# Optimization experiments

Measured on AMD Instinct MI355X. Metric: run time of the kernel, lower is better.

## Reference

```python
import jax, jax.numpy as jnp
import numpy as np


def setup_inputs() -> dict:
    key = jax.random.key(0)
    k1, k2, k3 = jax.random.split(key, 3)
    b, c, h, w = 4, 64, 64, 64
    content = jax.random.normal(k1, (b, c, h, w), dtype=jnp.float32)
    content_s = jax.random.normal(k2, (b, c, h, w), dtype=jnp.float32)
    style = jax.random.normal(k3, (b, c, h, w), dtype=jnp.float32)
    return {"content": content, "content_s": content_s, "style": style}


def reference(content, content_s, style):
    b, c, h, w = content.shape
    hw = h * w
    Fc = content.reshape(b, c, hw)      # [b, c, HW]
    Fs = content_s.reshape(b, c, hw)    # [b, c, HW]
    Fst = style.reshape(b, c, hw)       # [b, c, HW]
    # S[b, q, k] = sum_c Fc[b, c, q] * Fs[b, c, k]  (Fc transposed as in torch)
    S = jnp.einsum('bcq,bck->bqk', Fc, Fs)
    S = jax.nn.softmax(S, axis=-1)
    # O = style @ S^T : O[b, c, q] = sum_k Fst[b, c, k] * S[b, q, k]
    O = jnp.einsum('bck,bqk->bcq', Fst, S).reshape(b, c, h, w)
    return jnp.concatenate((content, O), axis=1)
```

## Files before the change

kernel.cpp:

```cpp
#include <hip/hip_runtime.h>
#include <math.h>


#define Bb 4
#define Cc 64
#define HWs 4096
#define SPLITS 4
#define TILES_PER_SPLIT 16
#define RLOG2E 1.44269504088896340736f

typedef _Float16 half8 __attribute__((ext_vector_type(8)));
typedef _Float16 half4 __attribute__((ext_vector_type(4)));
typedef float floatx4 __attribute__((ext_vector_type(4)));

__global__ __launch_bounds__(256) void prep_k(const float* __restrict__ content,
                                              const float* __restrict__ Fs,
                                              const float* __restrict__ Fst,
                                              float* __restrict__ out,
                                              _Float16* __restrict__ Kt,
                                              _Float16* __restrict__ Vt) {
    const int bid = blockIdx.x;
    const int t = threadIdx.x;
    if (bid < 1024) {
        int i4 = bid * 256 + t;
        const float4* c4 = (const float4*)content;
        const float4* v4 = (const float4*)Fst;
        float4* o4 = (float4*)out;
        int b = i4 >> 16, rem = i4 & 65535;
        o4[(size_t)b * 131072 + rem] = c4[i4];
        float4 v = v4[i4];
        half4 h;
        h[0] = (_Float16)v.x; h[1] = (_Float16)v.y;
        h[2] = (_Float16)v.z; h[3] = (_Float16)v.w;
        *(half4*)(Vt + (size_t)i4 * 4) = h;
    } else {
        __shared__ _Float16 T[16][72];
        int e = bid - 1024;
        int b = e >> 8;
        int hw0 = (e & 255) * 16;
        const float* sb = Fs + (size_t)b * Cc * HWs;
        {
            int c = t >> 2, x4 = (t & 3) * 4;
            float4 v = *(const float4*)(sb + (size_t)c * HWs + hw0 + x4);
            T[x4 + 0][c] = (_Float16)v.x;
            T[x4 + 1][c] = (_Float16)v.y;
            T[x4 + 2][c] = (_Float16)v.z;
            T[x4 + 3][c] = (_Float16)v.w;
        }
        __syncthreads();
        if (t < 128) {
            int row = t >> 3, g = t & 7;
            _Float16* db = Kt + (size_t)b * HWs * Cc;
            *(half8*)(db + (size_t)(hw0 + row) * Cc + g * 8) = *(half8*)&T[row][g * 8];
        }
    }
}

__global__ __launch_bounds__(256, 2) void attn_k(const float* __restrict__ Fc,
                                                 const _Float16* __restrict__ Kt,
                                                 const _Float16* __restrict__ Vt,
                                                 _Float16* __restrict__ Opart,
                                                 float2* __restrict__ ml) {
    const int tid  = threadIdx.x;
    const int w    = tid >> 6;
    const int lane = tid & 63;
    const int quad = lane >> 4;
    const int l15  = lane & 15;
    const int qg = blockIdx.x & 31;
    const int b  = (blockIdx.x >> 5) & 3;
    const int s  = blockIdx.x >> 7;
    const int k0base = s * TILES_PER_SPLIT * 64;
    const int qA = qg * 128 + w * 32 + l15;
    const int qB = qA + 16;

    __shared__ _Float16 Kl[2][64 * 64];
    __shared__ _Float16 Vl[2][64 * 64];
    __shared__ _Float16 Ps[4][32][72];

    const float*    Fcb = Fc + (size_t)b * Cc * HWs;
    const _Float16* Kb  = Kt + (size_t)b * HWs * Cc;
    const _Float16* Vb  = Vt + (size_t)b * Cc * HWs;

    const bool isK  = tid < 128;
    const int  sl   = tid & 127;
    const int  srow = sl >> 3;
    const int  sjg  = sl & 7;
    const int  ssw  = (sjg ^ (srow & 7)) * 8;

    half8 qf[2][2];
    #pragma unroll
    for (int j = 0; j < 8; ++j) {
        qf[0][0][j] = (_Float16)(Fcb[(size_t)(quad * 8 + j) * HWs + qA] * RLOG2E);
        qf[0][1][j] = (_Float16)(Fcb[(size_t)(32 + quad * 8 + j) * HWs + qA] * RLOG2E);
        qf[1][0][j] = (_Float16)(Fcb[(size_t)(quad * 8 + j) * HWs + qB] * RLOG2E);
        qf[1][1][j] = (_Float16)(Fcb[(size_t)(32 + quad * 8 + j) * HWs + qB] * RLOG2E);
    }

    half8 st[4];
    auto stage_load = [&](int kt) {
        int kk0 = k0base + kt * 64;
        #pragma unroll
        for (int i = 0; i < 4; ++i) {
            int row = srow + 16 * i;
            if (isK) st[i] = *(const half8*)(Kb + (size_t)(kk0 + row) * 64 + sjg * 8);
            else     st[i] = *(const half8*)(Vb + (size_t)row * HWs + kk0 + sjg * 8);
        }
    };
    auto stage_write = [&](int p) {
        #pragma unroll
        for (int i = 0; i < 4; ++i) {
            int row = srow + 16 * i;
            if (isK) *(half8*)&Kl[p][row * 64 + ssw] = st[i];
            else     *(half8*)&Vl[p][row * 64 + ssw] = st[i];
        }
    };

    floatx4 acc[2][4];
    #pragma unroll
    for (int g = 0; g < 2; ++g)
        #pragma unroll
        for (int m = 0; m < 4; ++m) acc[g][m] = (floatx4)(0.0f);
    float m_run[2] = {-INFINITY, -INFINITY};
    float lsum[2] = {0.0f, 0.0f};

    stage_load(0);
    stage_write(0);
    stage_load(1);
    __syncthreads();

    const int swl = (l15 & 7);
    for (int kt = 0; kt < TILES_PER_SPLIT; ++kt) {
        const int p = kt & 1;
        if (kt + 1 < TILES_PER_SPLIT) stage_write(p ^ 1);
        if (kt + 2 < TILES_PER_SPLIT) stage_load(kt + 2);

        half8 ka[4][2];
        #pragma unroll
        for (int m = 0; m < 4; ++m)
            #pragma unroll
            for (int cs = 0; cs < 2; ++cs)
                ka[m][cs] = *(const half8*)&Kl[p][(m * 16 + l15) * 64 + (((cs * 4 + quad) ^ swl) * 8)];

        floatx4 sv[2][4];
        #pragma unroll
        for (int m = 0; m < 4; ++m) {
            #pragma unroll
            for (int g = 0; g < 2; ++g) {
                sv[g][m] = __builtin_amdgcn_mfma_f32_16x16x32_f16(ka[m][0], qf[g][0], (floatx4)(0.0f), 0, 0, 0);
                sv[g][m] = __builtin_amdgcn_mfma_f32_16x16x32_f16(ka[m][1], qf[g][1], sv[g][m], 0, 0, 0);
            }
        }

        half8 va[4][2];
        #pragma unroll
        for (int m = 0; m < 4; ++m)
            #pragma unroll
            for (int ks = 0; ks < 2; ++ks)
                va[m][ks] = *(const half8*)&Vl[p][(m * 16 + l15) * 64 + (((ks * 4 + quad) ^ swl) * 8)];

        half8 pb[2][2];
        #pragma unroll
        for (int g = 0; g < 2; ++g) {
            float mx = -INFINITY;
            #pragma unroll
            for (int m = 0; m < 4; ++m)
                #pragma unroll
                for (int r = 0; r < 4; ++r) mx = fmaxf(mx, sv[g][m][r]);
            mx = fmaxf(mx, __shfl_xor(mx, 16));
            mx = fmaxf(mx, __shfl_xor(mx, 32));
            float m_new = fmaxf(m_run[g], mx);
            float alpha = exp2f(m_run[g] - m_new);
            m_run[g] = m_new;
            float part = 0.0f;
            #pragma unroll
            for (int m = 0; m < 4; ++m)
                #pragma unroll
                for (int r = 0; r < 4; ++r) {
                    float e = exp2f(sv[g][m][r] - m_new);
                    sv[g][m][r] = e;
                    part += e;
                }
            lsum[g] = lsum[g] * alpha + part;
            #pragma unroll
            for (int m = 0; m < 4; ++m)
                #pragma unroll
                for (int r = 0; r < 4; ++r) acc[g][m][r] *= alpha;

            #pragma unroll
            for (int m = 0; m < 4; ++m) {
                half4 pp;
                pp[0] = (_Float16)sv[g][m][0]; pp[1] = (_Float16)sv[g][m][1];
                pp[2] = (_Float16)sv[g][m][2]; pp[3] = (_Float16)sv[g][m][3];
                *(half4*)&Ps[w][g * 16 + l15][m * 16 + quad * 4] = pp;
            }
            pb[g][0] = *(half8*)&Ps[w][g * 16 + l15][quad * 8];
            pb[g][1] = *(half8*)&Ps[w][g * 16 + l15][32 + quad * 8];
        }

        #pragma unroll
        for (int m = 0; m < 4; ++m)
            #pragma unroll
            for (int g = 0; g < 2; ++g) {
                acc[g][m] = __builtin_amdgcn_mfma_f32_16x16x32_f16(va[m][0], pb[g][0], acc[g][m], 0, 0, 0);
                acc[g][m] = __builtin_amdgcn_mfma_f32_16x16x32_f16(va[m][1], pb[g][1], acc[g][m], 0, 0, 0);
            }

        __syncthreads();
    }

    _Float16* op = Opart + (((size_t)s * Bb + b) * Cc) * HWs;
    #pragma unroll
    for (int g = 0; g < 2; ++g) {
        lsum[g] += __shfl_xor(lsum[g], 16);
        lsum[g] += __shfl_xor(lsum[g], 32);
        int q = (g == 0) ? qA : qB;
        #pragma unroll
        for (int m = 0; m < 4; ++m)
            #pragma unroll
            for (int r = 0; r < 4; ++r) {
                int c = m * 16 + quad * 4 + r;
                op[(size_t)c * HWs + q] = (_Float16)acc[g][m][r];
            }
        if (quad == 0)
            ml[((size_t)b * HWs + q) * SPLITS + s] = make_float2(m_run[g], lsum[g]);
    }
}

__global__ __launch_bounds__(256) void combine_k(const _Float16* __restrict__ Opart,
                                                 const float2* __restrict__ ml,
                                                 float* __restrict__ out) {
    int idx = blockIdx.x * 256 + threadIdx.x;
    int q = idx & 4095;
    int c = (idx >> 12) & 63;
    int b = idx >> 18;
    const float2* mlp = ml + ((size_t)b * HWs + q) * SPLITS;
    float2 mls[SPLITS];
    #pragma unroll
    for (int s = 0; s < SPLITS; ++s) mls[s] = mlp[s];
    float M = -INFINITY;
    #pragma unroll
    for (int s = 0; s < SPLITS; ++s) M = fmaxf(M, mls[s].x);
    float l = 0.0f, wgt[SPLITS];
    #pragma unroll
    for (int s = 0; s < SPLITS; ++s) {
        wgt[s] = exp2f(mls[s].x - M);
        l += wgt[s] * mls[s].y;
    }
    float o = 0.0f;
    #pragma unroll
    for (int s = 0; s < SPLITS; ++s)
        o += wgt[s] * (float)Opart[(((size_t)s * Bb + b) * Cc + c) * HWs + q];
    out[((size_t)b * 2 * Cc + Cc + c) * HWs + q] = o / l;
}

extern "C" void kernel_launch(void* const* d_in, const int* in_sizes, int n_in,
                              void* d_out, int out_size, void* d_ws, size_t ws_size,
                              hipStream_t stream) {
    const float* content   = (const float*)d_in[0];
    const float* content_s = (const float*)d_in[1];
    const float* style     = (const float*)d_in[2];
    float* out = (float*)d_out;

    _Float16* Kt = (_Float16*)d_ws;
    _Float16* Vt = Kt + (size_t)Bb * HWs * Cc;
    _Float16* Opart = Vt + (size_t)Bb * Cc * HWs;
    float2*   ml = (float2*)(Opart + (size_t)SPLITS * Bb * Cc * HWs);

    prep_k<<<dim3(2048), dim3(256), 0, stream>>>(content, content_s, style, out, Kt, Vt);
    attn_k<<<dim3(SPLITS * Bb * 32), dim3(256), 0, stream>>>(content, Kt, Vt, Opart, ml);
    combine_k<<<dim3(4096), dim3(256), 0, stream>>>(Opart, ml, out);
}
```

Before: 109.1 us.

## Restructure flash-attention inner loop with lazy rescale, register P transpose, more splits

Removes the LDS round-trip for the probability tile by packing exp values to fp16 and transposing them with permlane32/permlane16 swaps. The running-max rescale is now skipped unless the max grows past a threshold, and the row sum is computed on the matrix cores by multiplying against a ones vector. Occupancy is raised to 4 blocks per SM and the key dimension is split into 8 pieces when the workspace is large enough. The intent is to cut ALU, LDS and sync overhead in the softmax. In exchange it adds more partial outputs for the combine kernel and relies on fp16 range holding under the deferred rescale.

Result: slower. 112.7 us, median of 2 (+3.2%).

```diff
diff --git a/kernel.cpp b/kernel.cpp
--- a/kernel.cpp
+++ b/kernel.cpp
@@ -5,13 +5,13 @@
 #define Bb 4
 #define Cc 64
 #define HWs 4096
-#define SPLITS 4
-#define TILES_PER_SPLIT 16
 #define RLOG2E 1.44269504088896340736f
+#define DEFER_THR 6.0f
 
 typedef _Float16 half8 __attribute__((ext_vector_type(8)));
 typedef _Float16 half4 __attribute__((ext_vector_type(4)));
 typedef float floatx4 __attribute__((ext_vector_type(4)));
+typedef unsigned uint2v __attribute__((ext_vector_type(2)));
 
 __global__ __launch_bounds__(256) void prep_k(const float* __restrict__ content,
                                               const float* __restrict__ Fs,
@@ -56,11 +56,13 @@
     }
 }
 
-__global__ __launch_bounds__(256, 2) void attn_k(const float* __restrict__ Fc,
+template <int NS>
+__global__ __launch_bounds__(256, 4) void attn_k(const float* __restrict__ Fc,
                                                  const _Float16* __restrict__ Kt,
                                                  const _Float16* __restrict__ Vt,
                                                  _Float16* __restrict__ Opart,
                                                  float2* __restrict__ ml) {
+    constexpr int TPS = 64 / NS;
     const int tid  = threadIdx.x;
     const int w    = tid >> 6;
     const int lane = tid & 63;
@@ -69,13 +71,12 @@
     const int qg = blockIdx.x & 31;
     const int b  = (blockIdx.x >> 5) & 3;
     const int s  = blockIdx.x >> 7;
-    const int k0base = s * TILES_PER_SPLIT * 64;
+    const int k0base = s * TPS * 64;
     const int qA = qg * 128 + w * 32 + l15;
     const int qB = qA + 16;
 
     __shared__ _Float16 Kl[2][64 * 64];
     __shared__ _Float16 Vl[2][64 * 64];
-    __shared__ _Float16 Ps[4][32][72];
 
     const float*    Fcb = Fc + (size_t)b * Cc * HWs;
     const _Float16* Kb  = Kt + (size_t)b * HWs * Cc;
@@ -116,12 +117,18 @@
     };
 
     floatx4 acc[2][4];
-    #pragma unroll
-    for (int g = 0; g < 2; ++g)
+    floatx4 accl[2];
+    #pragma unroll
+    for (int g = 0; g < 2; ++g) {
+        accl[g] = (floatx4)(0.0f);
         #pragma unroll
         for (int m = 0; m < 4; ++m) acc[g][m] = (floatx4)(0.0f);
+    }
     float m_run[2] = {-INFINITY, -INFINITY};
-    float lsum[2] = {0.0f, 0.0f};
+
+    half8 vone;
+    #pragma unroll
+    for (int j = 0; j < 8; ++j) vone[j] = (_Float16)1.0f;
 
     stage_load(0);
     stage_write(0);
@@ -129,90 +136,99 @@
     __syncthreads();
 
     const int swl = (l15 & 7);
-    for (int kt = 0; kt < TILES_PER_SPLIT; ++kt) {
+    for (int kt = 0; kt < TPS; ++kt) {
         const int p = kt & 1;
-        if (kt + 1 < TILES_PER_SPLIT) stage_write(p ^ 1);
-        if (kt + 2 < TILES_PER_SPLIT) stage_load(kt + 2);
-
-        half8 ka[4][2];
-        #pragma unroll
-        for (int m = 0; m < 4; ++m)
-            #pragma unroll
-            for (int cs = 0; cs < 2; ++cs)
-                ka[m][cs] = *(const half8*)&Kl[p][(m * 16 + l15) * 64 + (((cs * 4 + quad) ^ swl) * 8)];
+        if (kt + 1 < TPS) stage_write(p ^ 1);
+        if (kt + 2 < TPS) stage_load(kt + 2);
 
         floatx4 sv[2][4];
         #pragma unroll
         for (int m = 0; m < 4; ++m) {
-            #pragma unroll
-            for (int g = 0; g < 2; ++g) {
-                sv[g][m] = __builtin_amdgcn_mfma_f32_16x16x32_f16(ka[m][0], qf[g][0], (floatx4)(0.0f), 0, 0, 0);
-                sv[g][m] = __builtin_amdgcn_mfma_f32_16x16x32_f16(ka[m][1], qf[g][1], sv[g][m], 0, 0, 0);
-            }
-        }
-
-        half8 va[4][2];
-        #pragma unroll
-        for (int m = 0; m < 4; ++m)
-            #pragma unroll
-            for (int ks = 0; ks < 2; ++ks)
-                va[m][ks] = *(const half8*)&Vl[p][(m * 16 + l15) * 64 + (((ks * 4 + quad) ^ swl) * 8)];
+            const half8 ka0 = *(const half8*)&Kl[p][(m * 16 + l15) * 64 + ((quad ^ swl) * 8)];
+            const half8 ka1 = *(const half8*)&Kl[p][(m * 16 + l15) * 64 + (((4 + quad) ^ swl) * 8)];
+            sv[0][m] = __builtin_amdgcn_mfma_f32_16x16x32_f16(ka0, qf[0][0], (floatx4)(0.0f), 0, 0, 0);
+            sv[0][m] = __builtin_amdgcn_mfma_f32_16x16x32_f16(ka1, qf[0][1], sv[0][m], 0, 0, 0);
+            sv[1][m] = __builtin_amdgcn_mfma_f32_16x16x32_f16(ka0, qf[1][0], (floatx4)(0.0f), 0, 0, 0);
+            sv[1][m] = __builtin_amdgcn_mfma_f32_16x16x32_f16(ka1, qf[1][1], sv[1][m], 0, 0, 0);
+        }
 
         half8 pb[2][2];
         #pragma unroll
         for (int g = 0; g < 2; ++g) {
-            float mx = -INFINITY;
+            float mx = sv[g][0][0];
             #pragma unroll
             for (int m = 0; m < 4; ++m)
                 #pragma unroll
                 for (int r = 0; r < 4; ++r) mx = fmaxf(mx, sv[g][m][r]);
-            mx = fmaxf(mx, __shfl_xor(mx, 16));
-            mx = fmaxf(mx, __shfl_xor(mx, 32));
-            float m_new = fmaxf(m_run[g], mx);
-            float alpha = exp2f(m_run[g] - m_new);
-            m_run[g] = m_new;
-            float part = 0.0f;
-            #pragma unroll
-            for (int m = 0; m < 4; ++m)
+            {
+                unsigned mu = __float_as_uint(mx);
+                uint2v t32 = __builtin_amdgcn_permlane32_swap(mu, mu, false, false);
+                mx = fmaxf(__uint_as_float(t32[0]), __uint_as_float(t32[1]));
+                mu = __float_as_uint(mx);
+                uint2v t16 = __builtin_amdgcn_permlane16_swap(mu, mu, false, false);
+                mx = fmaxf(__uint_as_float(t16[0]), __uint_as_float(t16[1]));
+            }
+            if (!__all(mx - m_run[g] <= DEFER_THR)) {
+                float m_new = fmaxf(m_run[g], mx);
+                float alpha = exp2f(m_run[g] - m_new);
+                m_run[g] = m_new;
                 #pragma unroll
-                for (int r = 0; r < 4; ++r) {
-                    float e = exp2f(sv[g][m][r] - m_new);
-                    sv[g][m][r] = e;
-                    part += e;
-                }
-            lsum[g] = lsum[g] * alpha + part;
-            #pragma unroll
-            for (int m = 0; m < 4; ++m)
-                #pragma unroll
-                for (int r = 0; r < 4; ++r) acc[g][m][r] *= alpha;
-
+                for (int m = 0; m < 4; ++m) acc[g][m] *= alpha;
+                accl[g] *= alpha;
+            }
+            const float mb = m_run[g];
+            unsigned Ap[4], Bp[4];
             #pragma unroll
             for (int m = 0; m < 4; ++m) {
-                half4 pp;
-                pp[0] = (_Float16)sv[g][m][0]; pp[1] = (_Float16)sv[g][m][1];
-                pp[2] = (_Float16)sv[g][m][2]; pp[3] = (_Float16)sv[g][m][3];
-                *(half4*)&Ps[w][g * 16 + l15][m * 16 + quad * 4] = pp;
-            }
-            pb[g][0] = *(half8*)&Ps[w][g * 16 + l15][quad * 8];
-            pb[g][1] = *(half8*)&Ps[w][g * 16 + l15][32 + quad * 8];
-        }
-
-        #pragma unroll
-        for (int m = 0; m < 4; ++m)
-            #pragma unroll
-            for (int g = 0; g < 2; ++g) {
-                acc[g][m] = __builtin_amdgcn_mfma_f32_16x16x32_f16(va[m][0], pb[g][0], acc[g][m], 0, 0, 0);
-                acc[g][m] = __builtin_amdgcn_mfma_f32_16x16x32_f16(va[m][1], pb[g][1], acc[g][m], 0, 0, 0);
-            }
+                float e0 = exp2f(sv[g][m][0] - mb);
+                float e1 = exp2f(sv[g][m][1] - mb);
+                float e2 = exp2f(sv[g][m][2] - mb);
+                float e3 = exp2f(sv[g][m][3] - mb);
+                Ap[m] = __builtin_bit_cast(unsigned, __builtin_amdgcn_cvt_pkrtz(e0, e1));
+                Bp[m] = __builtin_bit_cast(unsigned, __builtin_amdgcn_cvt_pkrtz(e2, e3));
+            }
+            unsigned pw[2][4];
+            { uint2v a = __builtin_amdgcn_permlane32_swap(Ap[0], Ap[1], false, false);
+              uint2v u = __builtin_amdgcn_permlane16_swap(a[0], a[1], false, false);
+              pw[0][0] = u[0]; pw[0][2] = u[1]; }
+            { uint2v a = __builtin_amdgcn_permlane32_swap(Bp[0], Bp[1], false, false);
+              uint2v u = __builtin_amdgcn_permlane16_swap(a[0], a[1], false, false);
+              pw[0][1] = u[0]; pw[0][3] = u[1]; }
+            { uint2v a = __builtin_amdgcn_permlane32_swap(Ap[2], Ap[3], false, false);
+              uint2v u = __builtin_amdgcn_permlane16_swap(a[0], a[1], false, false);
+              pw[1][0] = u[0]; pw[1][2] = u[1]; }
+            { uint2v a = __builtin_amdgcn_permlane32_swap(Bp[2], Bp[3], false, false);
+              uint2v u = __builtin_amdgcn_permlane16_swap(a[0], a[1], false, false);
+              pw[1][1] = u[0]; pw[1][3] = u[1]; }
+            #pragma unroll
+            for (int ks = 0; ks < 2; ++ks) {
+                union { unsigned u4[4]; half8 h; } z;
+                z.u4[0] = pw[ks][0]; z.u4[1] = pw[ks][1];
+                z.u4[2] = pw[ks][2]; z.u4[3] = pw[ks][3];
+                pb[g][ks] = z.h;
+            }
+        }
+
+        #pragma unroll
+        for (int m = 0; m < 4; ++m) {
+            const half8 va0 = *(const half8*)&Vl[p][(m * 16 + l15) * 64 + ((quad ^ swl) * 8)];
+            const half8 va1 = *(const half8*)&Vl[p][(m * 16 + l15) * 64 + (((4 + quad) ^ swl) * 8)];
+            acc[0][m] = __builtin_amdgcn_mfma_f32_16x16x32_f16(va0, pb[0][0], acc[0][m], 0, 0, 0);
+            acc[0][m] = __builtin_amdgcn_mfma_f32_16x16x32_f16(va1, pb[0][1], acc[0][m], 0, 0, 0);
+            acc[1][m] = __builtin_amdgcn_mfma_f32_16x16x32_f16(va0, pb[1][0], acc[1][m], 0, 0, 0);
+            acc[1][m] = __builtin_amdgcn_mfma_f32_16x16x32_f16(va1, pb[1][1], acc[1][m], 0, 0, 0);
+        }
+        accl[0] = __builtin_amdgcn_mfma_f32_16x16x32_f16(vone, pb[0][0], accl[0], 0, 0, 0);
+        accl[0] = __builtin_amdgcn_mfma_f32_16x16x32_f16(vone, pb[0][1], accl[0], 0, 0, 0);
+        accl[1] = __builtin_amdgcn_mfma_f32_16x16x32_f16(vone, pb[1][0], accl[1], 0, 0, 0);
+        accl[1] = __builtin_amdgcn_mfma_f32_16x16x32_f16(vone, pb[1][1], accl[1], 0, 0, 0);
 
         __syncthreads();
     }
 
-    _Float16* op = Opart + (((size_t)s * Bb + b) * Cc) * HWs;
+    _Float16* op = Opart + ((size_t)(s * Bb + b) * Cc) * HWs;
     #pragma unroll
     for (int g = 0; g < 2; ++g) {
-        lsum[g] += __shfl_xor(lsum[g], 16);
-        lsum[g] += __shfl_xor(lsum[g], 32);
         int q = (g == 0) ? qA : qB;
         #pragma unroll
         for (int m = 0; m < 4; ++m)
@@ -222,10 +238,11 @@
                 op[(size_t)c * HWs + q] = (_Float16)acc[g][m][r];
             }
         if (quad == 0)
-            ml[((size_t)b * HWs + q) * SPLITS + s] = make_float2(m_run[g], lsum[g]);
-    }
-}
-
+            ml[((size_t)b * HWs + q) * NS + s] = make_float2(m_run[g], accl[g][0]);
+    }
+}
+
+template <int NS>
 __global__ __launch_bounds__(256) void combine_k(const _Float16* __restrict__ Opart,
                                                  const float2* __restrict__ ml,
                                                  float* __restrict__ out) {
@@ -233,23 +250,20 @@
     int q = idx & 4095;
     int c = (idx >> 12) & 63;
     int b = idx >> 18;
-    const float2* mlp = ml + ((size_t)b * HWs + q) * SPLITS;
-    float2 mls[SPLITS];
-    #pragma unroll
-    for (int s = 0; s < SPLITS; ++s) mls[s] = mlp[s];
+    const float2* mlp = ml + ((size_t)b * HWs + q) * NS;
+    float2 mls[NS];
+    #pragma unroll
+    for (int s = 0; s < NS; ++s) mls[s] = mlp[s];
     float M = -INFINITY;
     #pragma unroll
-    for (int s = 0; s < SPLITS; ++s) M = fmaxf(M, mls[s].x);
-    float l = 0.0f, wgt[SPLITS];
-    #pragma unroll
-    for (int s = 0; s < SPLITS; ++s) {
-        wgt[s] = exp2f(mls[s].x - M);
-        l += wgt[s] * mls[s].y;
-    }
-    float o = 0.0f;
-    #pragma unroll
-    for (int s = 0; s < SPLITS; ++s)
-        o += wgt[s] * (float)Opart[(((size_t)s * Bb + b) * Cc + c) * HWs + q];
+    for (int s = 0; s < NS; ++s) M = fmaxf(M, mls[s].x);
+    float l = 0.0f, o = 0.0f;
+    #pragma unroll
+    for (int s = 0; s < NS; ++s) {
+        float wgt = exp2f(mls[s].x - M);
+        l += wgt * mls[s].y;
+        o += wgt * (float)Opart[(((size_t)s * Bb + b) * Cc + c) * HWs + q];
+    }
     out[((size_t)b * 2 * Cc + Cc + c) * HWs + q] = o / l;
 }
 
@@ -264,9 +278,19 @@
     _Float16* Kt = (_Float16*)d_ws;
     _Float16* Vt = Kt + (size_t)Bb * HWs * Cc;
     _Float16* Opart = Vt + (size_t)Bb * Cc * HWs;
-    float2*   ml = (float2*)(Opart + (size_t)SPLITS * Bb * Cc * HWs);
+
+    const size_t base = (size_t)2 * Bb * HWs * Cc * sizeof(_Float16);
+    const size_t need8 = base + (size_t)8 * Bb * Cc * HWs * sizeof(_Float16)
+                              + (size_t)Bb * HWs * 8 * sizeof(float2);
+    const int ns = (ws_size >= need8) ? 8 : 4;
+    float2* ml = (float2*)(Opart + (size_t)ns * Bb * Cc * HWs);
 
     prep_k<<<dim3(2048), dim3(256), 0, stream>>>(content, content_s, style, out, Kt, Vt);
-    attn_k<<<dim3(SPLITS * Bb * 32), dim3(256), 0, stream>>>(content, Kt, Vt, Opart, ml);
-    combine_k<<<dim3(4096), dim3(256), 0, stream>>>(Opart, ml, out);
-}
+    if (ns == 8) {
+        attn_k<8><<<dim3(8 * Bb * 32), dim3(256), 0, stream>>>(content, Kt, Vt, Opart, ml);
+        combine_k<8><<<dim3(4096), dim3(256), 0, stream>>>(Opart, ml, out);
+    } else {
+        attn_k<4><<<dim3(4 * Bb * 32), dim3(256), 0, stream>>>(content, Kt, Vt, Opart, ml);
+        combine_k<4><<<dim3(4096), dim3(256), 0, stream>>>(Opart, ml, out);
+    }
+}
```
